# Performance work log

Measured on AMD Instinct MI355X. Metric: run time of the kernel, lower is better.

The kernel has to match this reference:

```python
import jax, jax.numpy as jnp
import numpy as np

B, L, E, H = 2, 2048, 1024, 16
D = E // H

def setup_inputs() -> dict:
    key = jax.random.key(0)
    ks = jax.random.split(key, 6)
    s = 1.0 / np.sqrt(E)
    return {
        "x": jax.random.normal(ks[0], (B, L, E), dtype=jnp.float32),
        "attention_mask": jnp.ones((B, L), dtype=jnp.float32),
        "Wq": jax.random.normal(ks[1], (E, E), dtype=jnp.float32) * s,
        "Wk": jax.random.normal(ks[2], (E, E), dtype=jnp.float32) * s,
        "Wv": jax.random.normal(ks[3], (E, E), dtype=jnp.float32) * s,
        "Wo": jax.random.normal(ks[4], (E, E), dtype=jnp.float32) * s,
        "bo": jnp.zeros((E,), dtype=jnp.float32),
    }

def reference(x, attention_mask, Wq, Wk, Wv, Wo, bo):
    b, l, e = x.shape
    h, d = H, D

    def proj(W):
        # (B,L,E) @ (E,E)^T -> (B,L,E) -> (B,H,L,D)
        return (x @ W.T).reshape(b, l, h, d).transpose(0, 2, 1, 3)

    q, k, v = proj(Wq), proj(Wk), proj(Wv)

    # multiplicative attention mask on q, k, v (mask shape (B,L) -> (B,1,L,1))
    m = attention_mask[:, None, :, None].astype(x.dtype)
    q, k, v = q * m, k * m, v * m

    scale = 1.0 / np.sqrt(d)
    scores = jnp.einsum('bhqd,bhkd->bhqk', q, k) * scale  # (B,H,L,L)
    causal = jnp.tril(jnp.ones((l, l), dtype=bool))
    scores = jnp.where(causal[None, None], scores, -jnp.inf)
    attn = jax.nn.softmax(scores, axis=-1)
    y = jnp.einsum('bhqk,bhkd->bhqd', attn, v)  # (B,H,L,D)
    y = y.transpose(0, 2, 1, 3).reshape(b, l, e)
    return y @ Wo.T + bo
```

## Files before the change

### kernel.cpp

```cpp
#include <hip/hip_runtime.h>
#include <cstdint>
#include <cstddef>
#include <math.h>

#define BB 2
#define LL 2048
#define EE 1024
#define HH 16
#define DD 64
#define MM (BB*LL)

typedef short short8 __attribute__((ext_vector_type(8)));
typedef float f32x4 __attribute__((ext_vector_type(4)));
typedef float f32x16 __attribute__((ext_vector_type(16)));

#define GPTR __attribute__((address_space(1)))
#define LPTR __attribute__((address_space(3)))

__device__ __forceinline__ unsigned short f32_bf16(float f) {
  union { float f; unsigned u; } c; c.f = f;
  c.u += 0x7fffu + ((c.u >> 16) & 1u);
  return (unsigned short)(c.u >> 16);
}

__device__ __forceinline__ unsigned pk_bf16(float lo, float hi) {
  unsigned r;
  asm("v_cvt_pk_bf16_f32 %0, %1, %2" : "=v"(r) : "v"(lo), "v"(hi));
  return r;
}
__device__ __forceinline__ void swap32(unsigned &a, unsigned &b) {
  asm("v_permlane32_swap_b32 %0, %1" : "+v"(a), "+v"(b));
}
__device__ __forceinline__ f32x16 zero16() {
  f32x16 v;
  #pragma unroll
  for (int e = 0; e < 16; ++e) v[e] = 0.f;
  return v;
}

__global__ void cvt_all(const float* __restrict__ x,  const float* __restrict__ wq,
                        const float* __restrict__ wk, const float* __restrict__ wv,
                        const float* __restrict__ wo,
                        unsigned short* __restrict__ xb,  unsigned short* __restrict__ wqb,
                        unsigned short* __restrict__ wkb, unsigned short* __restrict__ wvb,
                        unsigned short* __restrict__ wob)
{
  int i = (blockIdx.x * 256 + threadIdx.x) * 4;
  if (i >= MM * EE + 4 * EE * EE) return;
  const float* s; unsigned short* d; int off;
  if (i < MM * EE) { s = x; d = xb; off = i; }
  else {
    int k = i - MM * EE;
    int w = k >> 20;
    off = k & (EE * EE - 1);
    s = (w == 0) ? wq : (w == 1) ? wk : (w == 2) ? wv : wo;
    d = (w == 0) ? wqb : (w == 1) ? wkb : (w == 2) ? wvb : wob;
  }
  float4 v = *(const float4*)(s + off);
  union { unsigned short s[4]; uint2 u; } o;
  o.s[0] = f32_bf16(v.x); o.s[1] = f32_bf16(v.y);
  o.s[2] = f32_bf16(v.z); o.s[3] = f32_bf16(v.w);
  *(uint2*)(d + off) = o.u;
}

template<int MODE>
__global__ __launch_bounds__(256, 2)
void gemm128(const unsigned short* __restrict__ A,
             const unsigned short* __restrict__ W0,
             const unsigned short* __restrict__ W1,
             const unsigned short* __restrict__ W2,
             const float* __restrict__ mask,
             const float* __restrict__ bias,
             unsigned short* __restrict__ O0,
             unsigned short* __restrict__ O1,
             unsigned short* __restrict__ O2,
             float* __restrict__ OF)
{
  constexpr int K = EE;
  const int tid = threadIdx.x;
  const int lane = tid & 63;
  const int wid = tid >> 6;
  const int g = lane >> 4, li = lane & 15;
  const int m0 = blockIdx.y * 128;
  const int n0 = blockIdx.x * 128;
  const int z = blockIdx.z;

  const unsigned short* Wp = W0;
  if (MODE == 0) Wp = (z == 0) ? W0 : ((z == 1) ? W1 : W2);

  __shared__ unsigned short As[128 * 64];
  __shared__ unsigned short Bs[128 * 64];

  f32x4 acc[4][4];
  f32x4 zero = {0.f, 0.f, 0.f, 0.f};
  #pragma unroll
  for (int i = 0; i < 4; ++i)
    #pragma unroll
    for (int j = 0; j < 4; ++j) acc[i][j] = zero;

  const int wm = (wid >> 1) * 64;
  const int wn = (wid & 1) * 64;

  for (int kt = 0; kt < K; kt += 64) {
    #pragma unroll
    for (int j = 0; j < 4; ++j) {
      int c = j * 256 + tid;
      int row = c >> 3;
      int lcol = ((c & 7) * 16) ^ ((row & 7) << 4);
      __builtin_amdgcn_global_load_lds(
        (const GPTR void*)((const char*)(A + (size_t)(m0 + row) * K + kt) + lcol),
        (LPTR void*)((char*)As + c * 16), 16, 0, 0);
      __builtin_amdgcn_global_load_lds(
        (const GPTR void*)((const char*)(Wp + (size_t)(n0 + row) * K + kt) + lcol),
        (LPTR void*)((char*)Bs + c * 16), 16, 0, 0);
    }
    __syncthreads();

    #pragma unroll
    for (int kk = 0; kk < 2; ++kk) {
      short8 a[4], b[4];
      const int colb = (kk * 32 + g * 8) * 2;
      #pragma unroll
      for (int i = 0; i < 4; ++i) {
        int ar = wm + i * 16 + li;
        a[i] = *(const short8*)((const char*)As + ar * 128 + (colb ^ ((ar & 7) << 4)));
        int br = wn + i * 16 + li;
        b[i] = *(const short8*)((const char*)Bs + br * 128 + (colb ^ ((br & 7) << 4)));
      }
      #pragma unroll
      for (int i = 0; i < 4; ++i)
        #pragma unroll
        for (int j = 0; j < 4; ++j)
          acc[i][j] = __builtin_amdgcn_mfma_f32_16x16x32_bf16(a[i], b[j], acc[i][j], 0, 0, 0);
    }
    __syncthreads();
  }

  if (MODE == 0) {
    if (z == 2) {
      #pragma unroll
      for (int i = 0; i < 4; ++i) {
        int mbase = m0 + wm + i * 16 + g * 4;
        int bb2 = mbase >> 11;
        int l0  = mbase & (LL - 1);
        float mk[4];
        #pragma unroll
        for (int r = 0; r < 4; ++r) mk[r] = mask[mbase + r];
        #pragma unroll
        for (int j = 0; j < 4; ++j) {
          int n = n0 + wn + j * 16 + li;
          int h2 = n >> 6, dd2 = n & 63;
          union { unsigned short s[4]; uint2 u; } o;
          #pragma unroll
          for (int r = 0; r < 4; ++r) o.s[r] = f32_bf16(acc[i][j][r] * mk[r]);
          *(uint2*)(O2 + ((size_t)(bb2 * HH + h2) * DD + dd2) * LL + l0) = o.u;
        }
      }
    } else {
      unsigned short* Op = (z == 0) ? O0 : O1;
      const float sc = (z == 0) ? 0.125f : 1.0f;
      #pragma unroll
      for (int i = 0; i < 4; ++i) {
        #pragma unroll
        for (int r = 0; r < 4; ++r) {
          int m = m0 + wm + i * 16 + g * 4 + r;
          float mk = mask[m] * sc;
          int bb = m >> 11;
          int l  = m & (LL - 1);
          #pragma unroll
          for (int j = 0; j < 4; ++j) {
            int n = n0 + wn + j * 16 + li;
            int h = n >> 6, d = n & 63;
            size_t off = (((size_t)(bb * HH + h)) * LL + l) * DD + d;
            Op[off] = f32_bf16(acc[i][j][r] * mk);
          }
        }
      }
    }
  } else {
    #pragma unroll
    for (int i = 0; i < 4; ++i) {
      #pragma unroll
      for (int j = 0; j < 4; ++j) {
        int n = n0 + wn + j * 16 + li;
        float bv = bias[n];
        #pragma unroll
        for (int r = 0; r < 4; ++r) {
          int m = m0 + wm + i * 16 + g * 4 + r;
          OF[(size_t)m * EE + n] = acc[i][j][r] + bv;
        }
      }
    }
  }
}

__global__ __launch_bounds__(128, 2)
void attn2(const unsigned short* __restrict__ Q,
           const unsigned short* __restrict__ K,
           const unsigned short* __restrict__ VT,
           unsigned short* __restrict__ Y)
{
  const int tid = threadIdx.x, lane = tid & 63, wq = tid >> 6;
  const int l31 = lane & 31, hi = lane >> 5;

  const int id = blockIdx.x;
  const int bh_lo = id & 7;
  const int r_ = id >> 3;
  const int bh = (r_ & 3) * 8 + bh_lo;
  const int qt = 31 - (r_ >> 2);
  const int q0 = qt * 64;
  const int b = bh >> 4, h = bh & (HH - 1);
  const size_t kbase = (size_t)bh * LL * DD;

  __shared__ unsigned short Ks[2][64 * 64];
  __shared__ unsigned short Vs[2][64 * 64];

  const unsigned short* Kg  = K + kbase;
  const unsigned short* VTg = VT + kbase;

  const int qrow = q0 + wq * 32 + l31;
  const int qmin = q0 + wq * 32;

  short8 qf0, qf1, qf2, qf3;
  {
    const unsigned short* Qr = Q + kbase + (size_t)qrow * DD + hi * 8;
    qf0 = *(const short8*)(Qr);
    qf1 = *(const short8*)(Qr + 16);
    qf2 = *(const short8*)(Qr + 32);
    qf3 = *(const short8*)(Qr + 48);
  }

  f32x16 ot0 = zero16(), ot1 = zero16();
  float m = -INFINITY, lsum = 0.f;

  const int nt = qt + 1;

  auto stage = [&](int buf, int t2) {
    const int kv0s = t2 << 6;
    #pragma unroll
    for (int u = 0; u < 4; ++u) {
      int c = u * 128 + tid;
      int row = c >> 3;
      int cb = (c & 7) * 16;
      int scol = cb ^ ((row & 7) << 4);
      __builtin_amdgcn_global_load_lds(
        (const GPTR void*)((const char*)(Kg + (size_t)(kv0s + row) * DD) + scol),
        (LPTR void*)((char*)Ks[buf] + c * 16), 16, 0, 0);
      __builtin_amdgcn_global_load_lds(
        (const GPTR void*)((const char*)(VTg + (size_t)row * LL + kv0s) + scol),
        (LPTR void*)((char*)Vs[buf] + c * 16), 16, 0, 0);
    }
  };

  stage(0, 0);
  int cur = 0;

  for (int t = 0; t < nt; ++t) {
    __syncthreads();
    if (t + 1 < nt) stage(cur ^ 1, t + 1);
    const int kv0 = t << 6;
    const bool need1 = (kv0 + 32 <= qmin + 31);

    const char* Kb_ = (const char*)Ks[cur];
    const char* Vb_ = (const char*)Vs[cur];
    const int cb0 = hi * 16;
    const int r0 = l31, r1 = 32 + l31;
    const int swz = ((l31 & 7) << 4);

    f32x16 s0 = zero16(), s1 = zero16();
    __builtin_amdgcn_s_setprio(1);
    #pragma unroll
    for (int kc = 0; kc < 4; ++kc) {
      int cb = kc * 32 + cb0;
      short8 k0 = *(const short8*)(Kb_ + r0 * 128 + (cb ^ swz));
      short8 qv = (kc == 0) ? qf0 : (kc == 1) ? qf1 : (kc == 2) ? qf2 : qf3;
      s0 = __builtin_amdgcn_mfma_f32_32x32x16_bf16(k0, qv, s0, 0, 0, 0);
      if (need1) {
        short8 k1 = *(const short8*)(Kb_ + r1 * 128 + (cb ^ swz));
        s1 = __builtin_amdgcn_mfma_f32_32x32x16_bf16(k1, qv, s1, 0, 0, 0);
      }
    }
    __builtin_amdgcn_s_setprio(0);

    if (kv0 + 63 > qmin) {
      #pragma unroll
      for (int rg = 0; rg < 4; ++rg)
        #pragma unroll
        for (int e = 0; e < 4; ++e) {
          int kvg = kv0 + rg * 8 + hi * 4 + e;
          if (kvg > qrow)                s0[rg * 4 + e] = -INFINITY;
          if (need1 && kvg + 32 > qrow)  s1[rg * 4 + e] = -INFINITY;
        }
    }

    float red[16];
    #pragma unroll
    for (int e = 0; e < 16; ++e) red[e] = need1 ? fmaxf(s0[e], s1[e]) : s0[e];
    #pragma unroll
    for (int st = 8; st >= 1; st >>= 1)
      #pragma unroll
      for (int e = 0; e < 8; ++e) if (e < st) red[e] = fmaxf(red[e], red[e + st]);
    float mv = red[0];
    mv = fmaxf(mv, __shfl_xor(mv, 32, 64));

    if (!__all(mv <= m + 8.0f)) {
      float mnew = fmaxf(m, mv);
      float al = __expf(m - mnew);
      m = mnew;
      lsum *= al;
      #pragma unroll
      for (int e = 0; e < 16; ++e) { ot0[e] *= al; ot1[e] *= al; }
    }

    float rs;
    {
      float ra[16];
      #pragma unroll
      for (int e = 0; e < 16; ++e) { s0[e] = __expf(s0[e] - m); ra[e] = s0[e]; }
      if (need1) {
        #pragma unroll
        for (int e = 0; e < 16; ++e) { s1[e] = __expf(s1[e] - m); ra[e] += s1[e]; }
      }
      #pragma unroll
      for (int st = 8; st >= 1; st >>= 1)
        #pragma unroll
        for (int e = 0; e < 8; ++e) if (e < st) ra[e] += ra[e + st];
      rs = ra[0];
    }
    rs += __shfl_xor(rs, 32, 64);
    lsum += rs;

    auto mkfrag = [&](const f32x16& sv, int base) -> short8 {
      unsigned a0 = pk_bf16(sv[base + 0], sv[base + 1]);
      unsigned a1 = pk_bf16(sv[base + 2], sv[base + 3]);
      unsigned b0 = pk_bf16(sv[base + 4], sv[base + 5]);
      unsigned b1 = pk_bf16(sv[base + 6], sv[base + 7]);
      swap32(a0, b0);
      swap32(a1, b1);
      union { unsigned u[4]; short8 s; } f;
      f.u[0] = a0; f.u[1] = a1; f.u[2] = b0; f.u[3] = b1;
      return f.s;
    };
    short8 pf0 = mkfrag(s0, 0), pf1 = mkfrag(s0, 8);

    __builtin_amdgcn_s_setprio(1);
    #pragma unroll
    for (int kc = 0; kc < 2; ++kc) {
      int cb = kc * 32 + cb0;
      short8 v0 = *(const short8*)(Vb_ + r0 * 128 + (cb ^ swz));
      short8 v1 = *(const short8*)(Vb_ + r1 * 128 + (cb ^ swz));
      short8 pv = (kc == 0) ? pf0 : pf1;
      ot0 = __builtin_amdgcn_mfma_f32_32x32x16_bf16(v0, pv, ot0, 0, 0, 0);
      ot1 = __builtin_amdgcn_mfma_f32_32x32x16_bf16(v1, pv, ot1, 0, 0, 0);
    }
    __builtin_amdgcn_s_setprio(0);
    if (need1) {
      short8 pf2 = mkfrag(s1, 0), pf3 = mkfrag(s1, 8);
      __builtin_amdgcn_s_setprio(1);
      #pragma unroll
      for (int kc = 2; kc < 4; ++kc) {
        int cb = kc * 32 + cb0;
        short8 v0 = *(const short8*)(Vb_ + r0 * 128 + (cb ^ swz));
        short8 v1 = *(const short8*)(Vb_ + r1 * 128 + (cb ^ swz));
        short8 pv = (kc == 2) ? pf2 : pf3;
        ot0 = __builtin_amdgcn_mfma_f32_32x32x16_bf16(v0, pv, ot0, 0, 0, 0);
        ot1 = __builtin_amdgcn_mfma_f32_32x32x16_bf16(v1, pv, ot1, 0, 0, 0);
      }
      __builtin_amdgcn_s_setprio(0);
    }
    cur ^= 1;
  }

  float inv = 1.0f / lsum;
  unsigned short* Yr = Y + ((size_t)b * LL + qrow) * EE + h * DD;
  #pragma unroll
  for (int rg = 0; rg < 4; ++rg) {
    union { unsigned short s[4]; uint2 u; } o0, o1;
    #pragma unroll
    for (int e = 0; e < 4; ++e) {
      o0.s[e] = f32_bf16(ot0[rg * 4 + e] * inv);
      o1.s[e] = f32_bf16(ot1[rg * 4 + e] * inv);
    }
    *(uint2*)(Yr + rg * 8 + hi * 4) = o0.u;
    *(uint2*)(Yr + 32 + rg * 8 + hi * 4) = o1.u;
  }
}

extern "C" void kernel_launch(void* const* d_in, const int* in_sizes, int n_in,
                              void* d_out, int out_size, void* d_ws, size_t ws_size,
                              hipStream_t stream) {
  const float* x    = (const float*)d_in[0];
  const float* mask = (const float*)d_in[1];
  const float* Wq   = (const float*)d_in[2];
  const float* Wk   = (const float*)d_in[3];
  const float* Wv   = (const float*)d_in[4];
  const float* Wo   = (const float*)d_in[5];
  const float* bo   = (const float*)d_in[6];
  float* out = (float*)d_out;

  char* ws = (char*)d_ws;
  unsigned short* xb  = (unsigned short*)(ws);
  unsigned short* wqb = (unsigned short*)(ws + ((size_t)8  << 20));
  unsigned short* wkb = (unsigned short*)(ws + ((size_t)10 << 20));
  unsigned short* wvb = (unsigned short*)(ws + ((size_t)12 << 20));
  unsigned short* wob = (unsigned short*)(ws + ((size_t)14 << 20));
  unsigned short* Qb  = (unsigned short*)(ws + ((size_t)16 << 20));
  unsigned short* Kb  = (unsigned short*)(ws + ((size_t)24 << 20));
  unsigned short* VTb = (unsigned short*)(ws + ((size_t)32 << 20));
  unsigned short* Yb  = (unsigned short*)(ws + ((size_t)40 << 20));

  cvt_all<<<8192, 256, 0, stream>>>(x, Wq, Wk, Wv, Wo, xb, wqb, wkb, wvb, wob);

  gemm128<0><<<dim3(EE / 128, MM / 128, 3), 256, 0, stream>>>(
      xb, wqb, wkb, wvb, mask, nullptr, Qb, Kb, VTb, nullptr);

  attn2<<<dim3(1024), 128, 0, stream>>>(Qb, Kb, VTb, Yb);

  gemm128<1><<<dim3(EE / 128, MM / 128, 1), 256, 0, stream>>>(
      Yb, wob, nullptr, nullptr, nullptr, bo, nullptr, nullptr, nullptr, out);
}
```

Baseline: 121.9 us.

## Preload K/V LDS fragments into registers before staging; fold log2e into Q scale

At the start of each kv tile, the attention loop now reads all K and V fragments for the current buffer from LDS into registers. It then issues the async global-to-LDS prefetch for the next tile, with a sched_barrier between them. This lets the compute section run from registers and keeps LDS reads out of the MFMA chain. Separately, the Q projection scale now folds in log2(e), so the softmax can use exp2f instead of __expf. The costs are more vector registers (64 extra per lane for the fragments), which may reduce occupancy, and V fragments are loaded even when the diagonal tile only needs half of them.

```diff
diff --git a/kernel.cpp b/kernel.cpp
--- a/kernel.cpp
+++ b/kernel.cpp
@@ -158,7 +158,7 @@
       }
     } else {
       unsigned short* Op = (z == 0) ? O0 : O1;
-      const float sc = (z == 0) ? 0.125f : 1.0f;
+      const float sc = (z == 0) ? 0.125f * 1.44269504088896f : 1.0f;
       #pragma unroll
       for (int i = 0; i < 4; ++i) {
         #pragma unroll
@@ -221,13 +221,11 @@
   const int qrow = q0 + wq * 32 + l31;
   const int qmin = q0 + wq * 32;
 
-  short8 qf0, qf1, qf2, qf3;
+  short8 qf[4];
   {
     const unsigned short* Qr = Q + kbase + (size_t)qrow * DD + hi * 8;
-    qf0 = *(const short8*)(Qr);
-    qf1 = *(const short8*)(Qr + 16);
-    qf2 = *(const short8*)(Qr + 32);
-    qf3 = *(const short8*)(Qr + 48);
+    #pragma unroll
+    for (int kc = 0; kc < 4; ++kc) qf[kc] = *(const short8*)(Qr + kc * 16);
   }
 
   f32x16 ot0 = zero16(), ot1 = zero16();
@@ -255,30 +253,42 @@
   stage(0, 0);
   int cur = 0;
 
+  const int cb0 = hi * 16;
+  const int r0 = l31, r1 = 32 + l31;
+  const int swz = ((l31 & 7) << 4);
+
   for (int t = 0; t < nt; ++t) {
     __syncthreads();
+    const char* Kb_ = (const char*)Ks[cur];
+    const char* Vb_ = (const char*)Vs[cur];
+
+    short8 k0[4], k1[4], v0[4], v1[4];
+    #pragma unroll
+    for (int kc = 0; kc < 4; ++kc) {
+      int cb = (kc * 32 + cb0) ^ swz;
+      k0[kc] = *(const short8*)(Kb_ + r0 * 128 + cb);
+      k1[kc] = *(const short8*)(Kb_ + r1 * 128 + cb);
+      v0[kc] = *(const short8*)(Vb_ + r0 * 128 + cb);
+      v1[kc] = *(const short8*)(Vb_ + r1 * 128 + cb);
+    }
     if (t + 1 < nt) stage(cur ^ 1, t + 1);
+    __builtin_amdgcn_sched_barrier(0);
+
     const int kv0 = t << 6;
     const bool need1 = (kv0 + 32 <= qmin + 31);
 
-    const char* Kb_ = (const char*)Ks[cur];
-    const char* Vb_ = (const char*)Vs[cur];
-    const int cb0 = hi * 16;
-    const int r0 = l31, r1 = 32 + l31;
-    const int swz = ((l31 & 7) << 4);
-
     f32x16 s0 = zero16(), s1 = zero16();
     __builtin_amdgcn_s_setprio(1);
-    #pragma unroll
-    for (int kc = 0; kc < 4; ++kc) {
-      int cb = kc * 32 + cb0;
-      short8 k0 = *(const short8*)(Kb_ + r0 * 128 + (cb ^ swz));
-      short8 qv = (kc == 0) ? qf0 : (kc == 1) ? qf1 : (kc == 2) ? qf2 : qf3;
-      s0 = __builtin_amdgcn_mfma_f32_32x32x16_bf16(k0, qv, s0, 0, 0, 0);
-      if (need1) {
-        short8 k1 = *(const short8*)(Kb_ + r1 * 128 + (cb ^ swz));
-        s1 = __builtin_amdgcn_mfma_f32_32x32x16_bf16(k1, qv, s1, 0, 0, 0);
-      }
+    if (need1) {
+      #pragma unroll
+      for (int kc = 0; kc < 4; ++kc) {
+        s0 = __builtin_amdgcn_mfma_f32_32x32x16_bf16(k0[kc], qf[kc], s0, 0, 0, 0);
+        s1 = __builtin_amdgcn_mfma_f32_32x32x16_bf16(k1[kc], qf[kc], s1, 0, 0, 0);
+      }
+    } else {
+      #pragma unroll
+      for (int kc = 0; kc < 4; ++kc)
+        s0 = __builtin_amdgcn_mfma_f32_32x32x16_bf16(k0[kc], qf[kc], s0, 0, 0, 0);
     }
     __builtin_amdgcn_s_setprio(0);
 
@@ -305,7 +315,7 @@
 
     if (!__all(mv <= m + 8.0f)) {
       float mnew = fmaxf(m, mv);
-      float al = __expf(m - mnew);
+      float al = exp2f(m - mnew);
       m = mnew;
       lsum *= al;
       #pragma unroll
@@ -316,10 +326,10 @@
     {
       float ra[16];
       #pragma unroll
-      for (int e = 0; e < 16; ++e) { s0[e] = __expf(s0[e] - m); ra[e] = s0[e]; }
+      for (int e = 0; e < 16; ++e) { s0[e] = exp2f(s0[e] - m); ra[e] = s0[e]; }
       if (need1) {
         #pragma unroll
-        for (int e = 0; e < 16; ++e) { s1[e] = __expf(s1[e] - m); ra[e] += s1[e]; }
+        for (int e = 0; e < 16; ++e) { s1[e] = exp2f(s1[e] - m); ra[e] += s1[e]; }
       }
       #pragma unroll
       for (int st = 8; st >= 1; st >>= 1)
@@ -341,33 +351,25 @@
       f.u[0] = a0; f.u[1] = a1; f.u[2] = b0; f.u[3] = b1;
       return f.s;
     };
-    short8 pf0 = mkfrag(s0, 0), pf1 = mkfrag(s0, 8);
+    short8 pf[4];
+    pf[0] = mkfrag(s0, 0); pf[1] = mkfrag(s0, 8);
+    if (need1) { pf[2] = mkfrag(s1, 0); pf[3] = mkfrag(s1, 8); }
 
     __builtin_amdgcn_s_setprio(1);
-    #pragma unroll
-    for (int kc = 0; kc < 2; ++kc) {
-      int cb = kc * 32 + cb0;
-      short8 v0 = *(const short8*)(Vb_ + r0 * 128 + (cb ^ swz));
-      short8 v1 = *(const short8*)(Vb_ + r1 * 128 + (cb ^ swz));
-      short8 pv = (kc == 0) ? pf0 : pf1;
-      ot0 = __builtin_amdgcn_mfma_f32_32x32x16_bf16(v0, pv, ot0, 0, 0, 0);
-      ot1 = __builtin_amdgcn_mfma_f32_32x32x16_bf16(v1, pv, ot1, 0, 0, 0);
+    if (need1) {
+      #pragma unroll
+      for (int kc = 0; kc < 4; ++kc) {
+        ot0 = __builtin_amdgcn_mfma_f32_32x32x16_bf16(v0[kc], pf[kc], ot0, 0, 0, 0);
+        ot1 = __builtin_amdgcn_mfma_f32_32x32x16_bf16(v1[kc], pf[kc], ot1, 0, 0, 0);
+      }
+    } else {
+      #pragma unroll
+      for (int kc = 0; kc < 2; ++kc) {
+        ot0 = __builtin_amdgcn_mfma_f32_32x32x16_bf16(v0[kc], pf[kc], ot0, 0, 0, 0);
+        ot1 = __builtin_amdgcn_mfma_f32_32x32x16_bf16(v1[kc], pf[kc], ot1, 0, 0, 0);
+      }
     }
     __builtin_amdgcn_s_setprio(0);
-    if (need1) {
-      short8 pf2 = mkfrag(s1, 0), pf3 = mkfrag(s1, 8);
-      __builtin_amdgcn_s_setprio(1);
-      #pragma unroll
-      for (int kc = 2; kc < 4; ++kc) {
-        int cb = kc * 32 + cb0;
-        short8 v0 = *(const short8*)(Vb_ + r0 * 128 + (cb ^ swz));
-        short8 v1 = *(const short8*)(Vb_ + r1 * 128 + (cb ^ swz));
-        short8 pv = (kc == 2) ? pf2 : pf3;
-        ot0 = __builtin_amdgcn_mfma_f32_32x32x16_bf16(v0, pv, ot0, 0, 0, 0);
-        ot1 = __builtin_amdgcn_mfma_f32_32x32x16_bf16(v1, pv, ot1, 0, 0, 0);
-      }
-      __builtin_amdgcn_s_setprio(0);
-    }
     cur ^= 1;
   }
 
```

Measured after the change: 130.0 us. 1.07x slower.
